# Kernel tuning notes

Hardware: AMD Instinct MI355X
Metric: run time of the kernel (lower is better)

## Reference

```python
import jax, jax.numpy as jnp
import numpy as np

N_DIM = 1024
N_HEAD = 16
HEAD_DIM = N_DIM // N_HEAD  # 64
HALF = HEAD_DIM // 2        # 32, per-axis RoPE dim
BASE = 10000.0


def _rope_1d(x, pos, dim_h, base=BASE):
    # x: [B,H,S,dim_h], pos: [B,H,S] int
    theta = 1.0 / (base ** (jnp.arange(0, dim_h, 2, dtype=jnp.float32) / dim_h))  # [dim_h/2]
    pos_c = jnp.maximum(pos, 0)
    ang = pos_c[..., None].astype(jnp.float32) * theta  # [B,H,S,dim_h/2]
    cos, sin = jnp.cos(ang), jnp.sin(ang)
    xs = x.astype(jnp.float32).reshape(*x.shape[:-1], dim_h // 2, 2)
    x0, x1 = xs[..., 0], xs[..., 1]
    r0 = x0 * cos - x1 * sin
    r1 = x1 * cos + x0 * sin
    m = (pos >= 0)[..., None]  # [B,H,S,1]
    r0 = jnp.where(m, r0, x0)
    r1 = jnp.where(m, r1, x1)
    out = jnp.stack([r0, r1], axis=-1).reshape(x.shape)
    return out.astype(x.dtype)


def _rope_2d(x, positions):
    # x: [B,H,S,D], positions: [B,1,S,2] -> expand over heads
    B, H, S, D = x.shape
    pos = jnp.broadcast_to(positions, (B, H, S, 2))
    xh = _rope_1d(x[..., :HALF], pos[..., 0], HALF)
    xw = _rope_1d(x[..., HALF:], pos[..., 1], HALF)
    return jnp.concatenate([xh, xw], axis=-1)


def setup_inputs() -> dict:
    key = jax.random.key(0)
    k1, k2, k3, k4 = jax.random.split(key, 4)
    B, T = 8, 1024
    x = jax.random.normal(k1, (B, T, N_DIM), dtype=jnp.float32)
    attn_mask = jnp.ones((B, 1, T), dtype=bool)
    positions = jax.random.randint(k2, (B, T, 2), 0, 1024, dtype=jnp.int64)
    s = 1.0 / np.sqrt(N_DIM)
    w_qkv = jax.random.normal(k3, (N_DIM, 3 * N_DIM), dtype=jnp.float32) * s
    w_proj = jax.random.normal(k4, (N_DIM, N_DIM), dtype=jnp.float32) * s
    return {"x": x, "attn_mask": attn_mask, "positions": positions,
            "w_qkv": w_qkv, "w_proj": w_proj}


def reference(x, attn_mask, positions, w_qkv, w_proj):
    B, T, C = x.shape
    qkv = x @ w_qkv  # [B,T,3C]
    q, k, v = jnp.split(qkv, 3, axis=2)
    # -> [B,H,T,D]
    def to_heads(t):
        return t.reshape(B, T, N_HEAD, HEAD_DIM).transpose(0, 2, 1, 3)
    q, k, v = to_heads(q), to_heads(k), to_heads(v)
    pos = positions[:, None]  # [B,1,S,2]
    q = _rope_2d(q, pos)
    k = _rope_2d(k, pos)
    scale = 1.0 / np.sqrt(HEAD_DIM)
    scores = jnp.einsum("bhsd,bhtd->bhst", q, k) * scale  # [B,H,T,T]
    mask = attn_mask[:, None]  # [B,1,1,T]
    scores = jnp.where(mask, scores, jnp.float32(-1e30))
    attn = jax.nn.softmax(scores, axis=-1)
    out = jnp.einsum("bhst,bhtd->bhsd", attn, v)  # [B,H,T,D]
    out = out.transpose(0, 2, 1, 3).reshape(B, T, C)
    y = out @ w_proj
    return y
```

## Files before the change

kernel.cpp:

```cpp
#include <hip/hip_runtime.h>
#include <math.h>

#define BATCH 8
#define TSEQ 1024
#define NDIM 1024
#define NHEAD 16
#define HDIM 64
#define QKV_COLS 3072

#define QSCALE 0.18033688011112042f
#define DEFER_THR 10.0f

#define EXP2F(x) __builtin_amdgcn_exp2f(x)

typedef __attribute__((ext_vector_type(8))) short bf16x8;
typedef __attribute__((ext_vector_type(4))) float f32x4;

__device__ inline unsigned short f2bf(float x) {
    unsigned u = __float_as_uint(x);
    unsigned r = u + 0x7fffu + ((u >> 16) & 1u);
    return (unsigned short)(r >> 16);
}
__device__ inline float bf2f(unsigned short h) {
    return __uint_as_float(((unsigned)h) << 16);
}

__device__ inline void gl16(const unsigned short* g, unsigned short* l) {
    __builtin_amdgcn_global_load_lds(
        (const __attribute__((address_space(1))) unsigned int*)g,
        (__attribute__((address_space(3))) unsigned int*)l, 16, 0, 0);
}

template<int OUT_BF16>
__global__ __launch_bounds__(256)
void gemm_bf16k(const unsigned short* __restrict__ A,
                const unsigned short* __restrict__ BT,
                void* __restrict__ Cv, int M, int N, int K) {
    __shared__ unsigned short As[128 * 32];
    __shared__ unsigned short Bs[128 * 32];
    const int tid  = threadIdx.x;
    const int wave = tid >> 6, lane = tid & 63;
    const int row0 = blockIdx.y * 128, col0 = blockIdx.x * 128;
    const int wr = (wave >> 1) * 64, wc = (wave & 1) * 64;

    f32x4 acc[4][4] = {};

    const int srow = lane >> 2;
    const int scol = (lane & 3) * 8;
    const size_t abase = (size_t)row0 * K;
    const size_t bbase = (size_t)col0 * K;
    const int i0 = wave * 2;

    for (int kt = 0; kt < K; kt += 32) {
        __syncthreads();
        gl16(&A [abase + (size_t)(i0 * 16 + srow) * K + kt + scol], &As[i0 * 512]);
        gl16(&A [abase + (size_t)((i0 + 1) * 16 + srow) * K + kt + scol], &As[(i0 + 1) * 512]);
        gl16(&BT[bbase + (size_t)(i0 * 16 + srow) * K + kt + scol], &Bs[i0 * 512]);
        gl16(&BT[bbase + (size_t)((i0 + 1) * 16 + srow) * K + kt + scol], &Bs[(i0 + 1) * 512]);
        __syncthreads();

        bf16x8 a[4], b[4];
#pragma unroll
        for (int m = 0; m < 4; ++m)
            a[m] = *(const bf16x8*)&As[(wr + m * 16 + (lane & 15)) * 32 + (lane >> 4) * 8];
#pragma unroll
        for (int n = 0; n < 4; ++n)
            b[n] = *(const bf16x8*)&Bs[(wc + n * 16 + (lane & 15)) * 32 + (lane >> 4) * 8];
#pragma unroll
        for (int m = 0; m < 4; ++m)
#pragma unroll
            for (int n = 0; n < 4; ++n)
                acc[m][n] = __builtin_amdgcn_mfma_f32_16x16x32_bf16(
                                a[m], b[n], acc[m][n], 0, 0, 0);
    }

    const int crow = row0 + wr + (lane >> 4) * 4;
    const int ccol = col0 + wc + (lane & 15);
#pragma unroll
    for (int m = 0; m < 4; ++m)
#pragma unroll
        for (int n = 0; n < 4; ++n)
#pragma unroll
            for (int j = 0; j < 4; ++j) {
                size_t idx = (size_t)(crow + m * 16 + j) * N + ccol + n * 16;
                if (OUT_BF16) ((unsigned short*)Cv)[idx] = f2bf(acc[m][n][j]);
                else          ((float*)Cv)[idx] = acc[m][n][j];
            }
}

__global__ void detect_pos(const int* __restrict__ p, int* __restrict__ flag) {
    __shared__ int s_any;
    if (threadIdx.x == 0) s_any = 0;
    __syncthreads();
    int acc = 0;
    for (int i = 1 + 2 * (int)threadIdx.x; i < BATCH * TSEQ * 2; i += 512)
        acc |= p[i];
    if (acc) atomicOr(&s_any, 1);
    __syncthreads();
    if (threadIdx.x == 0) *flag = s_any;
}

__global__ void build_tab(float2* __restrict__ tab) {
    int i = blockIdx.x * 256 + threadIdx.x;
    int pos = i >> 4, f = i & 15;
    double theta = pow(10000.0, -(double)(2 * f) / 32.0);
    double s, c;
    sincos((double)pos * theta, &s, &c);
    tab[i] = make_float2((float)c, (float)s);
}

__global__ __launch_bounds__(256)
void cvt_x(const float* __restrict__ x, unsigned short* __restrict__ xb) {
    int i = blockIdx.x * 256 + threadIdx.x;
    float4 a = *(const float4*)(x + (size_t)i * 8);
    float4 b = *(const float4*)(x + (size_t)i * 8 + 4);
    unsigned short o[8] = { f2bf(a.x), f2bf(a.y), f2bf(a.z), f2bf(a.w),
                            f2bf(b.x), f2bf(b.y), f2bf(b.z), f2bf(b.w) };
    *(uint4*)(xb + (size_t)i * 8) = *(uint4*)o;
}

__global__ __launch_bounds__(256)
void transpose_w(const float* __restrict__ W, unsigned short* __restrict__ WT,
                 int K, int N) {
    __shared__ float Ls[16][68];
    const int n0 = blockIdx.x * 64, k0 = blockIdx.y * 16;
    const int t = threadIdx.x;
    {
        int kr = t >> 6, nn = t & 63;
#pragma unroll
        for (int j = 0; j < 4; ++j)
            Ls[kr * 4 + j][nn] = W[(size_t)(k0 + kr * 4 + j) * N + n0 + nn];
    }
    __syncthreads();
    {
        int r = t >> 2, c = (t & 3) * 4;
        unsigned short o[4];
#pragma unroll
        for (int j = 0; j < 4; ++j) o[j] = f2bf(Ls[c + j][r]);
        *(uint2*)&WT[(size_t)(n0 + r) * K + k0 + c] = *(uint2*)o;
    }
}

__global__ __launch_bounds__(256)
void rope_bf16(unsigned short* __restrict__ qkv,
               const int* __restrict__ positions,
               const int* __restrict__ flag,
               const float2* __restrict__ tab) {
    int g = blockIdx.x * 256 + threadIdx.x;
    int row = g >> 10, p = g & 1023;
    int tensor = p >> 9;
    int rr   = p & 511;
    int head = rr >> 5, pi = rr & 31;
    int half = pi >> 4, i = pi & 15;

    int stride = (*flag) ? 1 : 2;
    int pos = positions[(row * 2 + half) * stride];

    unsigned short* ptr = qkv + (size_t)row * QKV_COLS + tensor * NDIM +
                          head * HDIM + half * 32 + i * 2;
    unsigned pair = *(unsigned*)ptr;
    float x0 = bf2f((unsigned short)(pair & 0xffff));
    float x1 = bf2f((unsigned short)(pair >> 16));
    float c = 1.f, s = 0.f;
    if (pos >= 0) {
        float2 cs = tab[(pos < 1024 ? pos : 1023) * 16 + i];
        c = cs.x; s = cs.y;
    }
    float r0 = x0 * c - x1 * s;
    float r1 = x1 * c + x0 * s;
    if (tensor == 0) { r0 *= QSCALE; r1 *= QSCALE; }
    unsigned outp = (unsigned)f2bf(r0) | ((unsigned)f2bf(r1) << 16);
    *(unsigned*)ptr = outp;
}

__global__ __launch_bounds__(256)
void vtrans(const unsigned short* __restrict__ qkvb,
            unsigned short* __restrict__ VT) {
    __shared__ unsigned short Ls[64][72];
    const int blk = blockIdx.x;
    const int bh = blk >> 4, t0 = (blk & 15) * 64;
    const int b = bh >> 4, h = bh & 15;
    const int tid = threadIdx.x;
    {
        int r = tid >> 2, p4 = (tid & 3) * 16;
        const uint4* g = (const uint4*)(qkvb +
            (size_t)(b * TSEQ + t0 + r) * QKV_COLS + 2 * NDIM + h * HDIM + p4);
        uint4 v0 = g[0], v1 = g[1];
        *(uint4*)&Ls[r][p4] = v0;
        *(uint4*)&Ls[r][p4 + 8] = v1;
    }
    __syncthreads();
    {
        int d = tid >> 2, tc = tid & 3;
        unsigned short o[16];
#pragma unroll
        for (int j = 0; j < 16; ++j) o[j] = Ls[tc * 16 + j][d];
        unsigned short* dst = VT + ((size_t)bh * 64 + d) * TSEQ + t0 + tc * 16;
        *(uint4*)dst = *(uint4*)o;
        *(uint4*)(dst + 8) = *(uint4*)(o + 8);
    }
}

__global__ __launch_bounds__(256)
void attn_mfma3(const unsigned short* __restrict__ qkvb,
                const unsigned short* __restrict__ VT,
                unsigned short* __restrict__ out) {
    __shared__ unsigned short Kl[2][64 * 64];
    __shared__ unsigned short Vl[2][64 * 64];
    __shared__ unsigned short Ps[4][16][72];

    const int bh = blockIdx.x;
    const int b = bh >> 4, h = bh & 15;
    const int q0 = blockIdx.y * 64;
    const int tid = threadIdx.x, wave = tid >> 6, lane = tid & 63;
    const int lo = lane & 15, hi = lane >> 4;

    const size_t qrow_base = (size_t)b * TSEQ * QKV_COLS + h * HDIM;
    const unsigned short* Kg = qkvb + qrow_base + NDIM;
    const unsigned short* Vg = VT + (size_t)bh * HDIM * TSEQ;

    const int srow0  = wave * 16 + (lane >> 3);
    const int schunk = lane & 7;

    bf16x8 qf0, qf1;
    {
        const unsigned short* qp =
            qkvb + qrow_base + (size_t)(q0 + wave * 16 + lo) * QKV_COLS;
        qf0 = *(const bf16x8*)(qp + hi * 8);
        qf1 = *(const bf16x8*)(qp + 32 + hi * 8);
    }

#pragma unroll
    for (int j = 0; j < 2; ++j) {
        int rl = srow0 + j * 8;
        int sc = (schunk ^ (rl & 7)) * 8;
        gl16(Kg + (size_t)rl * QKV_COLS + sc, &Kl[0][(wave * 16 + j * 8) * 64]);
        gl16(Vg + (size_t)rl * TSEQ + sc,     &Vl[0][(wave * 16 + j * 8) * 64]);
    }
    __syncthreads();

    f32x4 Oacc[4] = {};
    float m = -1e30f;
    float l = 0.f;

    for (int kt = 0; kt < 16; ++kt) {
        const int cur = kt & 1;

        if (kt < 15) {
#pragma unroll
            for (int j = 0; j < 2; ++j) {
                int rl = srow0 + j * 8;
                int sc = (schunk ^ (rl & 7)) * 8;
                gl16(Kg + (size_t)((kt + 1) * 64 + rl) * QKV_COLS + sc,
                     &Kl[cur ^ 1][(wave * 16 + j * 8) * 64]);
                gl16(Vg + (size_t)rl * TSEQ + (kt + 1) * 64 + sc,
                     &Vl[cur ^ 1][(wave * 16 + j * 8) * 64]);
            }
        }

        f32x4 s[4] = {};
#pragma unroll
        for (int n = 0; n < 4; ++n) {
            int R = n * 16 + lo, sw = R & 7;
            bf16x8 k0 = *(const bf16x8*)&Kl[cur][R * 64 + ((hi ^ sw) << 3)];
            bf16x8 k1 = *(const bf16x8*)&Kl[cur][R * 64 + (((hi + 4) ^ sw) << 3)];
            s[n] = __builtin_amdgcn_mfma_f32_16x16x32_bf16(k0, qf0, s[n], 0, 0, 0);
            s[n] = __builtin_amdgcn_mfma_f32_16x16x32_bf16(k1, qf1, s[n], 0, 0, 0);
        }

        float pmax = -1e30f;
#pragma unroll
        for (int n = 0; n < 4; ++n)
#pragma unroll
            for (int j = 0; j < 4; ++j) pmax = fmaxf(pmax, s[n][j]);
        pmax = fmaxf(pmax, __shfl_xor(pmax, 16));
        pmax = fmaxf(pmax, __shfl_xor(pmax, 32));

        if (!__all(pmax <= m + DEFER_THR)) {
            float mnew  = fmaxf(m, pmax);
            float alpha = EXP2F(m - mnew);
            l *= alpha;
            m = mnew;
#pragma unroll
            for (int j = 0; j < 4; ++j) {
                float aj = __shfl(alpha, 4 * hi + j);
#pragma unroll
                for (int n = 0; n < 4; ++n) Oacc[n][j] *= aj;
            }
        }

        float rsum = 0.f;
#pragma unroll
        for (int n = 0; n < 4; ++n)
#pragma unroll
            for (int j = 0; j < 4; ++j) {
                float p = EXP2F(s[n][j] - m);
                s[n][j] = p;
                rsum += p;
            }
        rsum += __shfl_xor(rsum, 16);
        rsum += __shfl_xor(rsum, 32);
        l += rsum;

#pragma unroll
        for (int n = 0; n < 4; ++n) {
#pragma unroll
            for (int jp = 0; jp < 2; ++jp) {
                unsigned w = (unsigned)f2bf(s[n][2 * jp]) |
                             ((unsigned)f2bf(s[n][2 * jp + 1]) << 16);
                *(unsigned*)&Ps[wave][lo][16 * n + 4 * hi + 2 * jp] = w;
            }
        }
        bf16x8 pa0 = *(const bf16x8*)&Ps[wave][lo][8 * hi];
        bf16x8 pa1 = *(const bf16x8*)&Ps[wave][lo][32 + 8 * hi];

#pragma unroll
        for (int n = 0; n < 4; ++n) {
            int R = n * 16 + lo, sw = R & 7;
            bf16x8 v0 = *(const bf16x8*)&Vl[cur][R * 64 + ((hi ^ sw) << 3)];
            bf16x8 v1 = *(const bf16x8*)&Vl[cur][R * 64 + (((hi + 4) ^ sw) << 3)];
            Oacc[n] = __builtin_amdgcn_mfma_f32_16x16x32_bf16(pa0, v0, Oacc[n], 0, 0, 0);
            Oacc[n] = __builtin_amdgcn_mfma_f32_16x16x32_bf16(pa1, v1, Oacc[n], 0, 0, 0);
        }

        __syncthreads();
    }

#pragma unroll
    for (int j = 0; j < 4; ++j) {
        float inv = 1.f / __shfl(l, 4 * hi + j);
        int r = b * TSEQ + q0 + wave * 16 + 4 * hi + j;
#pragma unroll
        for (int n = 0; n < 4; ++n)
            out[(size_t)r * NDIM + h * HDIM + n * 16 + lo] =
                f2bf(Oacc[n][j] * inv);
    }
}

extern "C" void kernel_launch(void* const* d_in, const int* in_sizes, int n_in,
                              void* d_out, int out_size, void* d_ws, size_t ws_size,
                              hipStream_t stream) {
    (void)in_sizes; (void)n_in; (void)out_size; (void)ws_size;

    const float* x         = (const float*)d_in[0];
    const int*   positions = (const int*)d_in[2];
    const float* w_qkv     = (const float*)d_in[3];
    const float* w_proj    = (const float*)d_in[4];
    float* y = (float*)d_out;

    char* ws = (char*)d_ws;
    unsigned short* qkvb   = (unsigned short*)(ws);
    unsigned short* VT     = (unsigned short*)(ws + 50331648);
    unsigned short* aout   = (unsigned short*)(ws + 67108864);
    unsigned short* xb     = (unsigned short*)(ws + 83886080);
    unsigned short* wqkvT  = (unsigned short*)(ws + 100663296);
    unsigned short* wprojT = (unsigned short*)(ws + 106954752);
    float2*         tab    = (float2*)(ws + 109051904);
    int*            flag   = (int*)(ws + 109182976);

    detect_pos<<<1, 256, 0, stream>>>(positions, flag);
    build_tab<<<64, 256, 0, stream>>>(tab);
    cvt_x<<<(BATCH * TSEQ * NDIM / 8) / 256, 256, 0, stream>>>(x, xb);
    transpose_w<<<dim3(QKV_COLS / 64, NDIM / 16), 256, 0, stream>>>(w_qkv, wqkvT, NDIM, QKV_COLS);
    transpose_w<<<dim3(NDIM / 64, NDIM / 16), 256, 0, stream>>>(w_proj, wprojT, NDIM, NDIM);

    gemm_bf16k<1><<<dim3(QKV_COLS / 128, BATCH * TSEQ / 128), 256, 0, stream>>>(
        xb, wqkvT, qkvb, BATCH * TSEQ, QKV_COLS, NDIM);

    rope_bf16<<<(BATCH * TSEQ * 1024) / 256, 256, 0, stream>>>(qkvb, positions, flag, tab);

    vtrans<<<BATCH * NHEAD * (TSEQ / 64), 256, 0, stream>>>(qkvb, VT);

    attn_mfma3<<<dim3(BATCH * NHEAD, TSEQ / 64), 256, 0, stream>>>(qkvb, VT, aout);

    gemm_bf16k<0><<<dim3(NDIM / 128, BATCH * TSEQ / 128), 256, 0, stream>>>(
        aout, wprojT, y, BATCH * TSEQ, NDIM, NDIM);
}
```

Measured before the change: 227.1 us.

## Widen attention blocks to 128 queries with 8 waves sharing K/V tiles

The attention kernel now runs 512 threads per block covering 128 query rows, so each K/V tile loaded into shared memory serves twice as many queries. Each thread issues one async load per tile instead of two. The loop is unrolled by two with fixed double-buffer pointers. MFMA sections are wrapped in s_setprio, bf16 packing uses v_cvt_pk_bf16_f32, and the max reduction is rebalanced into a tree. Halving the block count may reduce occupancy and overlap, but global K/V traffic for the attention stage is cut in half.

```diff
diff --git a/kernel.cpp b/kernel.cpp
--- a/kernel.cpp
+++ b/kernel.cpp
@@ -201,17 +201,94 @@
     }
 }
 
-__global__ __launch_bounds__(256)
-void attn_mfma3(const unsigned short* __restrict__ qkvb,
+__device__ __forceinline__ void attn_tile(
+    const unsigned short* KB, const unsigned short* VB,
+    unsigned short* PsW,
+    const bf16x8& qf0, const bf16x8& qf1,
+    f32x4 (&Oacc)[4], float& m, float& l, int lo, int hi)
+{
+    f32x4 s[4] = {};
+    __builtin_amdgcn_s_setprio(1);
+#pragma unroll
+    for (int n = 0; n < 4; ++n) {
+        int R = n * 16 + lo, sw = R & 7;
+        bf16x8 k0 = *(const bf16x8*)&KB[R * 64 + ((hi ^ sw) << 3)];
+        bf16x8 k1 = *(const bf16x8*)&KB[R * 64 + (((hi + 4) ^ sw) << 3)];
+        s[n] = __builtin_amdgcn_mfma_f32_16x16x32_bf16(k0, qf0, s[n], 0, 0, 0);
+        s[n] = __builtin_amdgcn_mfma_f32_16x16x32_bf16(k1, qf1, s[n], 0, 0, 0);
+    }
+    __builtin_amdgcn_s_setprio(0);
+
+    float a0 = fmaxf(fmaxf(s[0][0], s[0][1]), s[0][2]);
+    float a1 = fmaxf(fmaxf(s[0][3], s[1][0]), s[1][1]);
+    float a2 = fmaxf(fmaxf(s[1][2], s[1][3]), s[2][0]);
+    float a3 = fmaxf(fmaxf(s[2][1], s[2][2]), s[2][3]);
+    float a4 = fmaxf(fmaxf(s[3][0], s[3][1]), s[3][2]);
+    float b0 = fmaxf(fmaxf(a0, a1), a2);
+    float b1 = fmaxf(fmaxf(a3, a4), s[3][3]);
+    float pmax = fmaxf(b0, b1);
+    pmax = fmaxf(pmax, __shfl_xor(pmax, 16));
+    pmax = fmaxf(pmax, __shfl_xor(pmax, 32));
+
+    if (!__all(pmax <= m + DEFER_THR)) {
+        float mnew  = fmaxf(m, pmax);
+        float alpha = EXP2F(m - mnew);
+        l *= alpha;
+        m = mnew;
+#pragma unroll
+        for (int j = 0; j < 4; ++j) {
+            float aj = __shfl(alpha, 4 * hi + j);
+#pragma unroll
+            for (int n = 0; n < 4; ++n) Oacc[n][j] *= aj;
+        }
+    }
+
+    float rsum = 0.f;
+#pragma unroll
+    for (int n = 0; n < 4; ++n)
+#pragma unroll
+        for (int j = 0; j < 4; ++j) {
+            float p = EXP2F(s[n][j] - m);
+            s[n][j] = p;
+            rsum += p;
+        }
+    rsum += __shfl_xor(rsum, 16);
+    rsum += __shfl_xor(rsum, 32);
+    l += rsum;
+
+#pragma unroll
+    for (int n = 0; n < 4; ++n) {
+        unsigned d0, d1;
+        asm("v_cvt_pk_bf16_f32 %0, %1, %2" : "=v"(d0) : "v"(s[n][0]), "v"(s[n][1]));
+        asm("v_cvt_pk_bf16_f32 %0, %1, %2" : "=v"(d1) : "v"(s[n][2]), "v"(s[n][3]));
+        *(uint2*)&PsW[lo * 72 + 16 * n + 4 * hi] = make_uint2(d0, d1);
+    }
+    bf16x8 pa0 = *(const bf16x8*)&PsW[lo * 72 + 8 * hi];
+    bf16x8 pa1 = *(const bf16x8*)&PsW[lo * 72 + 32 + 8 * hi];
+
+    __builtin_amdgcn_s_setprio(1);
+#pragma unroll
+    for (int n = 0; n < 4; ++n) {
+        int R = n * 16 + lo, sw = R & 7;
+        bf16x8 v0 = *(const bf16x8*)&VB[R * 64 + ((hi ^ sw) << 3)];
+        bf16x8 v1 = *(const bf16x8*)&VB[R * 64 + (((hi + 4) ^ sw) << 3)];
+        Oacc[n] = __builtin_amdgcn_mfma_f32_16x16x32_bf16(pa0, v0, Oacc[n], 0, 0, 0);
+        Oacc[n] = __builtin_amdgcn_mfma_f32_16x16x32_bf16(pa1, v1, Oacc[n], 0, 0, 0);
+    }
+    __builtin_amdgcn_s_setprio(0);
+}
+
+__global__ __launch_bounds__(512)
+void attn_mfma4(const unsigned short* __restrict__ qkvb,
                 const unsigned short* __restrict__ VT,
                 unsigned short* __restrict__ out) {
     __shared__ unsigned short Kl[2][64 * 64];
     __shared__ unsigned short Vl[2][64 * 64];
-    __shared__ unsigned short Ps[4][16][72];
+    __shared__ unsigned short Ps[8][16][72];
 
     const int bh = blockIdx.x;
     const int b = bh >> 4, h = bh & 15;
-    const int q0 = blockIdx.y * 64;
+    const int q0 = blockIdx.y * 128;
     const int tid = threadIdx.x, wave = tid >> 6, lane = tid & 63;
     const int lo = lane & 15, hi = lane >> 4;
 
@@ -219,8 +296,16 @@
     const unsigned short* Kg = qkvb + qrow_base + NDIM;
     const unsigned short* Vg = VT + (size_t)bh * HDIM * TSEQ;
 
-    const int srow0  = wave * 16 + (lane >> 3);
-    const int schunk = lane & 7;
+    const int srow   = tid >> 3;
+    const int schunk = tid & 7;
+    const int sc     = (schunk ^ (srow & 7)) * 8;
+    const unsigned short* kg0 = Kg + (size_t)srow * QKV_COLS + sc;
+    const unsigned short* vg0 = Vg + (size_t)srow * TSEQ + sc;
+    unsigned short* const kd0 = &Kl[0][(wave * 8) * 64];
+    unsigned short* const kd1 = &Kl[1][(wave * 8) * 64];
+    unsigned short* const vd0 = &Vl[0][(wave * 8) * 64];
+    unsigned short* const vd1 = &Vl[1][(wave * 8) * 64];
+    unsigned short* const PsW = &Ps[wave][0][0];
 
     bf16x8 qf0, qf1;
     {
@@ -230,99 +315,25 @@
         qf1 = *(const bf16x8*)(qp + 32 + hi * 8);
     }
 
-#pragma unroll
-    for (int j = 0; j < 2; ++j) {
-        int rl = srow0 + j * 8;
-        int sc = (schunk ^ (rl & 7)) * 8;
-        gl16(Kg + (size_t)rl * QKV_COLS + sc, &Kl[0][(wave * 16 + j * 8) * 64]);
-        gl16(Vg + (size_t)rl * TSEQ + sc,     &Vl[0][(wave * 16 + j * 8) * 64]);
-    }
+    gl16(kg0, kd0);
+    gl16(vg0, vd0);
     __syncthreads();
 
     f32x4 Oacc[4] = {};
     float m = -1e30f;
     float l = 0.f;
 
-    for (int kt = 0; kt < 16; ++kt) {
-        const int cur = kt & 1;
-
-        if (kt < 15) {
-#pragma unroll
-            for (int j = 0; j < 2; ++j) {
-                int rl = srow0 + j * 8;
-                int sc = (schunk ^ (rl & 7)) * 8;
-                gl16(Kg + (size_t)((kt + 1) * 64 + rl) * QKV_COLS + sc,
-                     &Kl[cur ^ 1][(wave * 16 + j * 8) * 64]);
-                gl16(Vg + (size_t)rl * TSEQ + (kt + 1) * 64 + sc,
-                     &Vl[cur ^ 1][(wave * 16 + j * 8) * 64]);
-            }
+    for (int kt = 0; kt < 16; kt += 2) {
+        gl16(kg0 + (size_t)(kt + 1) * 64 * QKV_COLS, kd1);
+        gl16(vg0 + (size_t)(kt + 1) * 64, vd1);
+        attn_tile(Kl[0], Vl[0], PsW, qf0, qf1, Oacc, m, l, lo, hi);
+        __syncthreads();
+
+        if (kt < 14) {
+            gl16(kg0 + (size_t)(kt + 2) * 64 * QKV_COLS, kd0);
+            gl16(vg0 + (size_t)(kt + 2) * 64, vd0);
         }
-
-        f32x4 s[4] = {};
-#pragma unroll
-        for (int n = 0; n < 4; ++n) {
-            int R = n * 16 + lo, sw = R & 7;
-            bf16x8 k0 = *(const bf16x8*)&Kl[cur][R * 64 + ((hi ^ sw) << 3)];
-            bf16x8 k1 = *(const bf16x8*)&Kl[cur][R * 64 + (((hi + 4) ^ sw) << 3)];
-            s[n] = __builtin_amdgcn_mfma_f32_16x16x32_bf16(k0, qf0, s[n], 0, 0, 0);
-            s[n] = __builtin_amdgcn_mfma_f32_16x16x32_bf16(k1, qf1, s[n], 0, 0, 0);
-        }
-
-        float pmax = -1e30f;
-#pragma unroll
-        for (int n = 0; n < 4; ++n)
-#pragma unroll
-            for (int j = 0; j < 4; ++j) pmax = fmaxf(pmax, s[n][j]);
-        pmax = fmaxf(pmax, __shfl_xor(pmax, 16));
-        pmax = fmaxf(pmax, __shfl_xor(pmax, 32));
-
-        if (!__all(pmax <= m + DEFER_THR)) {
-            float mnew  = fmaxf(m, pmax);
-            float alpha = EXP2F(m - mnew);
-            l *= alpha;
-            m = mnew;
-#pragma unroll
-            for (int j = 0; j < 4; ++j) {
-                float aj = __shfl(alpha, 4 * hi + j);
-#pragma unroll
-                for (int n = 0; n < 4; ++n) Oacc[n][j] *= aj;
-            }
-        }
-
-        float rsum = 0.f;
-#pragma unroll
-        for (int n = 0; n < 4; ++n)
-#pragma unroll
-            for (int j = 0; j < 4; ++j) {
-                float p = EXP2F(s[n][j] - m);
-                s[n][j] = p;
-                rsum += p;
-            }
-        rsum += __shfl_xor(rsum, 16);
-        rsum += __shfl_xor(rsum, 32);
-        l += rsum;
-
-#pragma unroll
-        for (int n = 0; n < 4; ++n) {
-#pragma unroll
-            for (int jp = 0; jp < 2; ++jp) {
-                unsigned w = (unsigned)f2bf(s[n][2 * jp]) |
-                             ((unsigned)f2bf(s[n][2 * jp + 1]) << 16);
-                *(unsigned*)&Ps[wave][lo][16 * n + 4 * hi + 2 * jp] = w;
-            }
-        }
-        bf16x8 pa0 = *(const bf16x8*)&Ps[wave][lo][8 * hi];
-        bf16x8 pa1 = *(const bf16x8*)&Ps[wave][lo][32 + 8 * hi];
-
-#pragma unroll
-        for (int n = 0; n < 4; ++n) {
-            int R = n * 16 + lo, sw = R & 7;
-            bf16x8 v0 = *(const bf16x8*)&Vl[cur][R * 64 + ((hi ^ sw) << 3)];
-            bf16x8 v1 = *(const bf16x8*)&Vl[cur][R * 64 + (((hi + 4) ^ sw) << 3)];
-            Oacc[n] = __builtin_amdgcn_mfma_f32_16x16x32_bf16(pa0, v0, Oacc[n], 0, 0, 0);
-            Oacc[n] = __builtin_amdgcn_mfma_f32_16x16x32_bf16(pa1, v1, Oacc[n], 0, 0, 0);
-        }
-
+        attn_tile(Kl[1], Vl[1], PsW, qf0, qf1, Oacc, m, l, lo, hi);
         __syncthreads();
     }
 
@@ -371,7 +382,7 @@
 
     vtrans<<<BATCH * NHEAD * (TSEQ / 64), 256, 0, stream>>>(qkvb, VT);
 
-    attn_mfma3<<<dim3(BATCH * NHEAD, TSEQ / 64), 256, 0, stream>>>(qkvb, VT, aout);
+    attn_mfma4<<<dim3(BATCH * NHEAD, TSEQ / 128), 512, 0, stream>>>(qkvb, VT, aout);
 
     gemm_bf16k<0><<<dim3(NDIM / 128, BATCH * TSEQ / 128), 256, 0, stream>>>(
         aout, wprojT, y, BATCH * TSEQ, NDIM, NDIM);
```

After: 208.7 us. -8.1%, faster.
